# Kernel tuning notes

Measured on AMD Instinct MI355X. Metric: run time of the kernel, lower is better.

The kernel has to match this reference:

```python
import jax, jax.numpy as jnp
import numpy as np

V, E = 50000, 300          # vocab, embedding dim (Word2Vec)
U1, U2, DNS = 256, 256, 128  # lstm1 units, lstm2 units, dense units
B, S = 64, 512             # batch, seq_len


def _glorot(key, shape):
    fan_in, fan_out = shape
    lim = jnp.sqrt(6.0 / (fan_in + fan_out))
    return jax.random.uniform(key, shape, jnp.float32, -lim, lim)


def setup_inputs() -> dict:
    key = jax.random.key(0)
    ks = jax.random.split(key, 12)
    d = {
        'tokens': jax.random.randint(ks[0], (B, S), 0, V),
        'emb': jax.random.normal(ks[1], (V, E), jnp.float32) * 0.05,
        # layer 1 gates: combined dim = E + U1
        'W1f': _glorot(ks[2], (E + U1, U1)), 'b1f': jnp.zeros((U1,), jnp.float32),
        'W1i': _glorot(ks[3], (E + U1, U1)), 'b1i': jnp.zeros((U1,), jnp.float32),
        'W1c': _glorot(ks[4], (E + U1, U1)), 'b1c': jnp.zeros((U1,), jnp.float32),
        'W1o': _glorot(ks[5], (E + U1, U1)), 'b1o': jnp.zeros((U1,), jnp.float32),
        # layer 2 gates: combined dim = U1 + U2
        'W2f': _glorot(ks[6], (U1 + U2, U2)), 'b2f': jnp.zeros((U2,), jnp.float32),
        'W2i': _glorot(ks[7], (U1 + U2, U2)), 'b2i': jnp.zeros((U2,), jnp.float32),
        'W2c': _glorot(ks[8], (U1 + U2, U2)), 'b2c': jnp.zeros((U2,), jnp.float32),
        'W2o': _glorot(ks[9], (U1 + U2, U2)), 'b2o': jnp.zeros((U2,), jnp.float32),
        'Wd': _glorot(ks[10], (U2, DNS)), 'bd': jnp.zeros((DNS,), jnp.float32),
        'Wout': _glorot(ks[11], (DNS, 1)), 'bout': jnp.zeros((1,), jnp.float32),
    }
    return d


def _lstm(x_seq, Wf, bf, Wi, bi, Wc, bc, Wo, bo, units):
    # x_seq: [B, S, D]; scan over time, returns all hidden states [B, S, units]
    b = x_seq.shape[0]
    h0 = jnp.zeros((b, units), x_seq.dtype)
    c0 = jnp.zeros((b, units), x_seq.dtype)

    def step(carry, x_t):
        h, c = carry
        z = jnp.concatenate([x_t, h], axis=-1)           # [B, D+units]
        f = jax.nn.sigmoid(z @ Wf + bf)
        i = jax.nn.sigmoid(z @ Wi + bi)
        g = jnp.tanh(z @ Wc + bc)
        c_new = f * c + i * g
        o = jax.nn.sigmoid(z @ Wo + bo)
        h_new = o * jnp.tanh(c_new)
        return (h_new, c_new), h_new

    (_, _), hs = jax.lax.scan(step, (h0, c0), jnp.swapaxes(x_seq, 0, 1))
    return jnp.swapaxes(hs, 0, 1)  # [B, S, units]


def reference(tokens, emb, W1f, b1f, W1i, b1i, W1c, b1c, W1o, b1o,
              W2f, b2f, W2i, b2i, W2c, b2c, W2o, b2o, Wd, bd, Wout, bout):
    x = emb[tokens]                                       # [B, S, E]
    h1 = _lstm(x, W1f, b1f, W1i, b1i, W1c, b1c, W1o, b1o, U1)   # [B, S, U1]
    h2 = _lstm(h1, W2f, b2f, W2i, b2i, W2c, b2c, W2o, b2o, U2)  # [B, S, U2]
    last = h2[:, -1, :]                                   # return_sequences=False -> final h
    d = jax.nn.relu(last @ Wd + bd)
    return jax.nn.sigmoid(d @ Wout + bout)                # [B, 1]
```

## Files before the change

### kernel.cpp

```cpp
#include <hip/hip_runtime.h>
#include <stdint.h>

typedef __bf16 bf16_t;
typedef __bf16 bf16x8 __attribute__((ext_vector_type(8)));
typedef float floatx16 __attribute__((ext_vector_type(16)));
typedef unsigned int u32;
typedef unsigned long long u64;

#define NPROD 64
#define H1R   8
#define SST   592
#define ZST   1104
#define FP    32

struct KParams {
  const int* tok;
  const float* emb;
  const float* W1[4]; const float* b1[4];
  const float* W2[4]; const float* b2[4];
  const float* Wd; const float* bd; const float* Wout; const float* bout;
  float* out;
  uint16_t* h1;
  uint16_t* h2;
  u32* fl0;
  u32* fl1;
  u32* fl0g;
  u32* pflags;
  float* dstage;
  bf16_t* w1bf;
  float* gx;
  int R;
};

__device__ __forceinline__ float sigf(float x) { return 1.f / (1.f + __expf(-x)); }
__device__ __forceinline__ float tanhf_fast(float x) { return 1.f - 2.f / (__expf(2.f * x) + 1.f); }

__device__ __forceinline__ u32 pack2(float a, float b) {
  uint16_t x = __builtin_bit_cast(uint16_t, (bf16_t)a);
  uint16_t y = __builtin_bit_cast(uint16_t, (bf16_t)b);
  return ((u32)y << 16) | (u32)x;
}
__device__ __forceinline__ float2 u2f2(u64 v) { union { u64 u; float2 f; } x; x.u = v; return x.f; }

__device__ __forceinline__ u32  ald32(const u32* p) { return __hip_atomic_load(p, __ATOMIC_RELAXED, __HIP_MEMORY_SCOPE_AGENT); }
__device__ __forceinline__ void ast32(u32* p, u32 v) { __hip_atomic_store(p, v, __ATOMIC_RELAXED, __HIP_MEMORY_SCOPE_AGENT); }
__device__ __forceinline__ u64  ald64(const u64* p) { return __hip_atomic_load(p, __ATOMIC_RELAXED, __HIP_MEMORY_SCOPE_AGENT); }

template<int NA, int NB>
__device__ __forceinline__ void waitcond(const u32* fa, u32 na, const u32* fb, u32 nb,
                                         const u32* pc, u32 nc) {
  const int lane = threadIdx.x & 63;
  const u32* ap; u32 need;
  if (lane < NA)           { ap = fa + lane * FP;        need = na; }
  else if (lane < NA + NB) { ap = fb + (lane - NA) * FP; need = nb; }
  else                     { ap = pc;                    need = nc; }
  while (!__all(ald32(ap) >= need)) {}
  __atomic_signal_fence(__ATOMIC_ACQUIRE);
}

__device__ __forceinline__ void waitg16(const u32* fa, u32 na) {
  const int lane = threadIdx.x & 63;
  const u32* ap = fa + (lane & 15) * FP;
  while (!__all(ald32(ap) >= na)) {}
  __atomic_signal_fence(__ATOMIC_ACQUIRE);
}

__device__ __forceinline__ void stage_h64(const u64* hp, char* smem) {
  const int tid = threadIdx.x;
  u64 tmp[16];
#pragma unroll
  for (int t = 0; t < 16; ++t) tmp[t] = ald64(hp + tid + 256 * t);
#pragma unroll
  for (int t = 0; t < 16; ++t) {
    int i = tid + 256 * t, b = i >> 6, cc = i & 63;
    *(u64*)(smem + b * SST + cc * 8) = tmp[t];
  }
}

__device__ void run_l0(const KParams& p, int sub, char* abuf, float* cst, float* biasl)
{
  const int tid = threadIdx.x;
  const int w = tid >> 6, l = tid & 63, q = l >> 5, lr = l & 31;
  const int mh = w & 1, nh = w >> 1;

  if (tid < 64) biasl[tid] = p.b1[tid >> 4][sub * 16 + (tid & 15)];

  const int c = nh * 32 + lr;
  const float* Wg = p.W1[c >> 4];
  const int un = sub * 16 + (c & 15);
  bf16x8 wf[16];
#pragma unroll
  for (int s = 0; s < 16; ++s)
#pragma unroll
    for (int j = 0; j < 8; ++j) {
      int k = 16 * s + 8 * q + j;
      wf[s][j] = (bf16_t)Wg[(300 + k) * 256 + un];
    }
  __syncthreads();

  float cs[2][2] = {{0.f, 0.f}, {0.f, 0.f}};

  for (int s = 0; s < 512; ++s) {
    u32 n1 = (s >= 8) ? (u32)(s - 7) : 0u;
    if (w == 0) waitcond<16, 32>(p.fl0, (u32)s, p.fl1, n1, &p.pflags[s * FP], 1u);
    __syncthreads();

    const float* slab = p.gx + (size_t)(s % p.R) * 65536u;
    u64 g[2][4];
#pragma unroll
    for (int kk = 0; kk < 2; ++kk) {
      int pp = tid + 256 * kk, b = pp >> 3, u2 = (pp & 7) * 2;
      const float* gb = slab + b * 1024 + sub * 64 + u2;
      g[kk][0] = ald64((const u64*)gb);
      g[kk][1] = ald64((const u64*)(gb + 16));
      g[kk][2] = ald64((const u64*)(gb + 32));
      g[kk][3] = ald64((const u64*)(gb + 48));
    }
    stage_h64((const u64*)(p.h1 + ((s + H1R - 1) & (H1R - 1)) * 16384), abuf);
    __syncthreads();

    floatx16 acc;
#pragma unroll
    for (int e = 0; e < 16; ++e) acc[e] = 0.f;
    const char* arow = abuf + (mh * 32 + lr) * SST + q * 16;
#pragma unroll
    for (int s2 = 0; s2 < 16; ++s2) {
      bf16x8 af = *(const bf16x8*)(arow + 32 * s2);
      acc = __builtin_amdgcn_mfma_f32_32x32x16_bf16(af, wf[s2], acc, 0, 0, 0);
    }
#pragma unroll
    for (int e = 0; e < 16; ++e) {
      int ri = (e & 3) + 8 * (e >> 2) + 4 * q;
      cst[(mh * 32 + ri) * 68 + nh * 32 + lr] = acc[e];
    }
    __syncthreads();

    uint16_t* hout = p.h1 + (s & (H1R - 1)) * 16384;
#pragma unroll
    for (int kk = 0; kk < 2; ++kk) {
      int pp = tid + 256 * kk, b = pp >> 3, u2 = (pp & 7) * 2;
      float2 pf = *(float2*)&cst[b * 68 +      u2];
      float2 pi = *(float2*)&cst[b * 68 + 16 + u2];
      float2 pg = *(float2*)&cst[b * 68 + 32 + u2];
      float2 po = *(float2*)&cst[b * 68 + 48 + u2];
      float2 gf = u2f2(g[kk][0]), gi = u2f2(g[kk][1]);
      float2 gg = u2f2(g[kk][2]), go = u2f2(g[kk][3]);
      float hv[2];
#pragma unroll
      for (int j = 0; j < 2; ++j) {
        float fj = sigf((j ? pf.y : pf.x) + (j ? gf.y : gf.x) + biasl[u2 + j]);
        float ij = sigf((j ? pi.y : pi.x) + (j ? gi.y : gi.x) + biasl[16 + u2 + j]);
        float gj = tanhf_fast((j ? pg.y : pg.x) + (j ? gg.y : gg.x) + biasl[32 + u2 + j]);
        float oj = sigf((j ? po.y : po.x) + (j ? go.y : go.x) + biasl[48 + u2 + j]);
        float cn = fj * cs[kk][j] + ij * gj;
        cs[kk][j] = cn;
        hv[j] = oj * tanhf_fast(cn);
      }
      ast32((u32*)(hout + b * 256 + sub * 16 + u2), pack2(hv[0], hv[1]));
    }
    __syncthreads();
    if (tid == 0) {
      ast32(&p.fl0[sub * FP], (u32)(s + 1));
      ast32(&p.fl0g[sub * FP], (u32)(s + 1));
    }
  }
}

__device__ void run_l1(const KParams& p, int w2, char* zbuf, float* cst, float* biasl)
{
  const int tid = threadIdx.x;
  const int wv = tid >> 6, l = tid & 63, q = l >> 5, lr = l & 31;
  const int nh = wv & 1, kh = wv >> 1;
  const int bh = w2 & 1, sub1 = w2 >> 1;

  if (tid < 64) biasl[tid] = p.b2[tid >> 4][sub1 * 16 + (tid & 15)];

  const int c = nh * 32 + lr;
  const float* Wg = p.W2[c >> 4];
  const int un = sub1 * 16 + (c & 15);
  bf16x8 wf[16];
#pragma unroll
  for (int s = 0; s < 16; ++s)
#pragma unroll
    for (int j = 0; j < 8; ++j) {
      int k = kh * 256 + s * 16 + q * 8 + j;
      wf[s][j] = (bf16_t)Wg[k * 256 + un];
    }
  __syncthreads();

  float cs2[2] = {0.f, 0.f};
  const int cb = tid >> 3, cu = (tid & 7) * 2;

  for (int s = 0; s < 512; ++s) {
    if (wv == 0) waitcond<32, 16>(p.fl1, (u32)s, p.fl0, (u32)(s + 1), p.fl0, 0u);
    __syncthreads();

    const u64* hp1 = (const u64*)(p.h1 + (s & (H1R - 1)) * 16384) + bh * 2048;
    const u64* hp2 = (const u64*)(p.h2 + ((s + 1) & 1) * 16384) + bh * 2048;
    u64 t1[8], t2[8];
#pragma unroll
    for (int t = 0; t < 8; ++t) t1[t] = ald64(hp1 + tid + 256 * t);
#pragma unroll
    for (int t = 0; t < 8; ++t) t2[t] = ald64(hp2 + tid + 256 * t);
#pragma unroll
    for (int t = 0; t < 8; ++t) {
      int i = tid + 256 * t, r = i >> 6, cc = i & 63;
      *(u64*)(zbuf + r * ZST + cc * 8) = t1[t];
    }
#pragma unroll
    for (int t = 0; t < 8; ++t) {
      int i = tid + 256 * t, r = i >> 6, cc = i & 63;
      *(u64*)(zbuf + r * ZST + 512 + cc * 8) = t2[t];
    }
    __syncthreads();

    floatx16 acc;
#pragma unroll
    for (int e = 0; e < 16; ++e) acc[e] = 0.f;
    const char* arow = zbuf + lr * ZST + kh * 512 + q * 16;
#pragma unroll
    for (int s2 = 0; s2 < 16; ++s2) {
      bf16x8 af = *(const bf16x8*)(arow + 32 * s2);
      acc = __builtin_amdgcn_mfma_f32_32x32x16_bf16(af, wf[s2], acc, 0, 0, 0);
    }
#pragma unroll
    for (int e = 0; e < 16; ++e) {
      int ri = (e & 3) + 8 * (e >> 2) + 4 * q;
      cst[kh * 2176 + ri * 68 + nh * 32 + lr] = acc[e];
    }
    __syncthreads();

    uint16_t* hout = p.h2 + (s & 1) * 16384;
    {
      float2 pf = *(float2*)&cst[cb * 68 +      cu];
      float2 pi = *(float2*)&cst[cb * 68 + 16 + cu];
      float2 pg = *(float2*)&cst[cb * 68 + 32 + cu];
      float2 po = *(float2*)&cst[cb * 68 + 48 + cu];
      float2 qf = *(float2*)&cst[2176 + cb * 68 +      cu];
      float2 qi = *(float2*)&cst[2176 + cb * 68 + 16 + cu];
      float2 qg = *(float2*)&cst[2176 + cb * 68 + 32 + cu];
      float2 qo = *(float2*)&cst[2176 + cb * 68 + 48 + cu];
      float hv[2];
#pragma unroll
      for (int j = 0; j < 2; ++j) {
        float fj = sigf((j ? pf.y + qf.y : pf.x + qf.x) + biasl[cu + j]);
        float ij = sigf((j ? pi.y + qi.y : pi.x + qi.x) + biasl[16 + cu + j]);
        float gj = tanhf_fast((j ? pg.y + qg.y : pg.x + qg.x) + biasl[32 + cu + j]);
        float oj = sigf((j ? po.y + qo.y : po.x + qo.x) + biasl[48 + cu + j]);
        float cn = fj * cs2[j] + ij * gj;
        cs2[j] = cn;
        hv[j] = oj * tanhf_fast(cn);
      }
      ast32((u32*)(hout + (bh * 32 + cb) * 256 + sub1 * 16 + cu), pack2(hv[0], hv[1]));
    }
    __syncthreads();
    if (tid == 0) ast32(&p.fl1[w2 * FP], (u32)(s + 1));
  }

  if (wv == 0) waitcond<32, 0>(p.fl1, 512u, p.fl1, 0u, p.fl1, 0u);
  __syncthreads();
  {
    const u64* hp = (const u64*)(p.h2 + 16384);
    u64 tmp[16];
#pragma unroll
    for (int t = 0; t < 16; ++t) tmp[t] = ald64(hp + tid + 256 * t);
#pragma unroll
    for (int t = 0; t < 16; ++t) {
      int i = tid + 256 * t, b = i >> 6, cc = i & 63;
      *(u64*)(zbuf + b * 520 + cc * 8) = tmp[t];
    }
  }
  __syncthreads();
  {
    int b = tid >> 2, cc = w2 * 4 + (tid & 3);
    const bf16_t* hrow = (const bf16_t*)(zbuf + b * 520);
    float a = p.bd[cc];
#pragma unroll 8
    for (int k = 0; k < 256; ++k) a += (float)hrow[k] * p.Wd[k * 128 + cc];
    ast32((u32*)&p.dstage[b * 128 + cc], __builtin_bit_cast(u32, fmaxf(a, 0.f)));
  }
  __syncthreads();
  if (tid == 0) ast32(&p.fl1[w2 * FP], 513u);

  if (w2 == 0) {
    if (wv == 0) waitcond<32, 0>(p.fl1, 513u, p.fl1, 0u, p.fl1, 0u);
    __syncthreads();
    if (tid < 64) {
      float a = p.bout[0];
#pragma unroll 8
      for (int cc = 0; cc < 128; ++cc) {
        u32 dv = ald32((u32*)&p.dstage[tid * 128 + cc]);
        a += __builtin_bit_cast(float, dv) * p.Wout[cc];
      }
      p.out[tid] = sigf(a);
    }
  }
}

__device__ void run_prod(const KParams& p, int pw, char* smem)
{
  const int tid = threadIdx.x;
  const int w = tid >> 6, l = tid & 63, q = l >> 5, lr = l & 31;
  const int mh = w & 1, chalf = w >> 1;
  const int R = p.R;

  for (int jj = 0; jj < 512 / NPROD; ++jj) {
    const int s = pw + NPROD * jj;
    if (s >= R) {
      if (w == 0) waitg16(p.fl0g, (u32)(s - R + 1));
    }
    __syncthreads();
    {
      int b = tid >> 2, qq = tid & 3;
      int tokv = p.tok[b * 512 + s];
      const float4* src = (const float4*)(p.emb + (size_t)tokv * 300);
      char* dst = smem + b * 656;
      for (int j2 = qq; j2 < 75; j2 += 4) {
        float4 v = src[j2];
        *(u32*)(dst + 8 * j2)     = pack2(v.x, v.y);
        *(u32*)(dst + 8 * j2 + 4) = pack2(v.z, v.w);
      }
      for (int i = tid; i < 640; i += 256) {
        int bb = i / 10, cc2 = i % 10;
        *(u32*)(smem + bb * 656 + 600 + cc2 * 4) = 0u;
      }
    }
    __syncthreads();

    bf16x8 afr[20];
    const char* arow = smem + (mh * 32 + lr) * 656 + q * 16;
#pragma unroll
    for (int kt = 0; kt < 20; ++kt) afr[kt] = *(const bf16x8*)(arow + 32 * kt);

    float* slab = p.gx + (size_t)(s % R) * 65536u;
    for (int c2 = 0; c2 < 16; ++c2) {
      int n = (chalf * 16 + c2) * 32 + lr;
      floatx16 acc;
#pragma unroll
      for (int e = 0; e < 16; ++e) acc[e] = 0.f;
#pragma unroll
      for (int kt = 0; kt < 20; ++kt) {
        bf16x8 bf = ((const bf16x8*)p.w1bf)[(kt * 1024 + n) * 2 + q];
        acc = __builtin_amdgcn_mfma_f32_32x32x16_bf16(afr[kt], bf, acc, 0, 0, 0);
      }
#pragma unroll
      for (int e = 0; e < 16; ++e) {
        int ri = (e & 3) + 8 * (e >> 2) + 4 * q;
        ast32((u32*)(slab + (mh * 32 + ri) * 1024 + n), __builtin_bit_cast(u32, acc[e]));
      }
    }
    __syncthreads();
    if (tid == 0) ast32(&p.pflags[s * FP], 1u);
  }
}

__global__ __launch_bounds__(256, 1) void lstm_main(KParams p)
{
  __shared__ __align__(16) char smem[64 * 656];
  __shared__ float cst[4352];
  __shared__ float biasl[64];
  const int wg = blockIdx.x;
  if (wg < 16)       run_l0(p, wg, smem, cst, biasl);
  else if (wg < 48)  run_l1(p, wg - 16, smem, cst, biasl);
  else               run_prod(p, wg - 48, smem);
}

__global__ void prep_w(KParams p) {
  int idx = blockIdx.x * 256 + threadIdx.x;
  if (idx >= 20 * 1024 * 16) return;
  int kk = idx & 15, n = (idx >> 4) & 1023, kt = idx >> 14;
  int k = kt * 16 + kk;
  int g = (n >> 4) & 3, su = n >> 6, u = n & 15;
  float v = (k < 300) ? p.W1[g][k * 256 + su * 16 + u] : 0.f;
  p.w1bf[idx] = (bf16_t)v;
}

__global__ void init_ws(u32* ws32) {
  int i = blockIdx.x * 256 + threadIdx.x;
  if (i < 100352) ws32[i] = 0u;
}

extern "C" void kernel_launch(void* const* d_in, const int* in_sizes, int n_in,
                              void* d_out, int out_size, void* d_ws, size_t ws_size,
                              hipStream_t stream)
{
  KParams p;
  p.tok = (const int*)d_in[0];
  p.emb = (const float*)d_in[1];
  for (int g = 0; g < 4; ++g) {
    p.W1[g] = (const float*)d_in[2 + 2 * g];
    p.b1[g] = (const float*)d_in[3 + 2 * g];
    p.W2[g] = (const float*)d_in[10 + 2 * g];
    p.b2[g] = (const float*)d_in[11 + 2 * g];
  }
  p.Wd   = (const float*)d_in[18];
  p.bd   = (const float*)d_in[19];
  p.Wout = (const float*)d_in[20];
  p.bout = (const float*)d_in[21];
  p.out  = (float*)d_out;

  char* ws = (char*)d_ws;
  p.h1     = (uint16_t*)ws;
  p.h2     = (uint16_t*)(ws + 262144);
  p.fl0    = (u32*)(ws + 327680);
  p.fl1    = (u32*)(ws + 329728);
  p.fl0g   = (u32*)(ws + 333824);
  p.pflags = (u32*)(ws + 335872);
  p.dstage = (float*)(ws + 401408);
  p.w1bf   = (bf16_t*)(ws + 434176);
  p.gx     = (float*)(ws + 1089536);

  long avail = (long)ws_size - 1089536L;
  int R = (int)(avail / 262144L);
  if (R > 64) R = 64;
  if (R < 1)  R = 1;
  p.R = R;

  hipLaunchKernelGGL(init_ws, dim3(392), dim3(256), 0, stream, (u32*)d_ws);
  hipLaunchKernelGGL(prep_w, dim3(1280), dim3(256), 0, stream, p);
  hipLaunchKernelGGL(lstm_main, dim3(16 + 32 + NPROD), dim3(256), 0, stream, p);
}
```

Baseline: 1.842 ms.

## Load MFMA A-fragments directly from global and store gx in fragment layout

The recurrent LSTM workgroups no longer stage h1/h2 through shared memory. Each lane now loads its own MFMA A-fragment straight from global memory, which removes a staging pass and a barrier per timestep. The producer now writes gate pre-activations in MFMA accumulator order using 64-bit stores, so layer 0 can add them and the bias directly into the accumulator. The h1 ring grows from 8 to 16 slots, which loosens the coupling between layer 0 and layer 1, at the cost of more workspace and redundant uncoalesced global reads per wave.

Result: slower. 3.592 ms (+95.0%).

```diff
diff --git a/kernel.cpp b/kernel.cpp
--- a/kernel.cpp
+++ b/kernel.cpp
@@ -8,9 +8,7 @@
 typedef unsigned long long u64;
 
 #define NPROD 64
-#define H1R   8
-#define SST   592
-#define ZST   1104
+#define H1R   16
 #define FP    32
 
 struct KParams {
@@ -41,10 +39,15 @@
   return ((u32)y << 16) | (u32)x;
 }
 __device__ __forceinline__ float2 u2f2(u64 v) { union { u64 u; float2 f; } x; x.u = v; return x.f; }
+__device__ __forceinline__ u64 f22u(float a, float b) { union { u64 u; float2 f; } x; x.f = make_float2(a, b); return x.u; }
+__device__ __forceinline__ bf16x8 mk_frag(u64 lo, u64 hi) {
+  union { u64 u[2]; bf16x8 v; } x; x.u[0] = lo; x.u[1] = hi; return x.v;
+}
 
 __device__ __forceinline__ u32  ald32(const u32* p) { return __hip_atomic_load(p, __ATOMIC_RELAXED, __HIP_MEMORY_SCOPE_AGENT); }
 __device__ __forceinline__ void ast32(u32* p, u32 v) { __hip_atomic_store(p, v, __ATOMIC_RELAXED, __HIP_MEMORY_SCOPE_AGENT); }
 __device__ __forceinline__ u64  ald64(const u64* p) { return __hip_atomic_load(p, __ATOMIC_RELAXED, __HIP_MEMORY_SCOPE_AGENT); }
+__device__ __forceinline__ void ast64(u64* p, u64 v) { __hip_atomic_store(p, v, __ATOMIC_RELAXED, __HIP_MEMORY_SCOPE_AGENT); }
 
 template<int NA, int NB>
 __device__ __forceinline__ void waitcond(const u32* fa, u32 na, const u32* fb, u32 nb,
@@ -65,29 +68,16 @@
   __atomic_signal_fence(__ATOMIC_ACQUIRE);
 }
 
-__device__ __forceinline__ void stage_h64(const u64* hp, char* smem) {
-  const int tid = threadIdx.x;
-  u64 tmp[16];
-#pragma unroll
-  for (int t = 0; t < 16; ++t) tmp[t] = ald64(hp + tid + 256 * t);
-#pragma unroll
-  for (int t = 0; t < 16; ++t) {
-    int i = tid + 256 * t, b = i >> 6, cc = i & 63;
-    *(u64*)(smem + b * SST + cc * 8) = tmp[t];
-  }
-}
-
-__device__ void run_l0(const KParams& p, int sub, char* abuf, float* cst, float* biasl)
+__device__ void run_l0(const KParams& p, int sub, float* cst)
 {
   const int tid = threadIdx.x;
   const int w = tid >> 6, l = tid & 63, q = l >> 5, lr = l & 31;
   const int mh = w & 1, nh = w >> 1;
 
-  if (tid < 64) biasl[tid] = p.b1[tid >> 4][sub * 16 + (tid & 15)];
-
   const int c = nh * 32 + lr;
   const float* Wg = p.W1[c >> 4];
   const int un = sub * 16 + (c & 15);
+  const float bias = p.b1[c >> 4][un];
   bf16x8 wf[16];
 #pragma unroll
   for (int s = 0; s < 16; ++s)
@@ -96,37 +86,40 @@
       int k = 16 * s + 8 * q + j;
       wf[s][j] = (bf16_t)Wg[(300 + k) * 256 + un];
     }
-  __syncthreads();
 
   float cs[2][2] = {{0.f, 0.f}, {0.f, 0.f}};
+  const int arow64 = (mh * 32 + lr) * 64 + q * 2;
 
   for (int s = 0; s < 512; ++s) {
-    u32 n1 = (s >= 8) ? (u32)(s - 7) : 0u;
-    if (w == 0) waitcond<16, 32>(p.fl0, (u32)s, p.fl1, n1, &p.pflags[s * FP], 1u);
-    __syncthreads();
-
-    const float* slab = p.gx + (size_t)(s % p.R) * 65536u;
-    u64 g[2][4];
-#pragma unroll
-    for (int kk = 0; kk < 2; ++kk) {
-      int pp = tid + 256 * kk, b = pp >> 3, u2 = (pp & 7) * 2;
-      const float* gb = slab + b * 1024 + sub * 64 + u2;
-      g[kk][0] = ald64((const u64*)gb);
-      g[kk][1] = ald64((const u64*)(gb + 16));
-      g[kk][2] = ald64((const u64*)(gb + 32));
-      g[kk][3] = ald64((const u64*)(gb + 48));
-    }
-    stage_h64((const u64*)(p.h1 + ((s + H1R - 1) & (H1R - 1)) * 16384), abuf);
-    __syncthreads();
+    u32 n1 = (s >= H1R) ? (u32)(s - (H1R - 1)) : 0u;
+    if (w == 0) waitcond<16, 16>(p.fl0, (u32)s, p.fl1, n1, &p.pflags[s * FP], 1u);
+    __syncthreads();
+
+    const u64* hp = (const u64*)(p.h1 + ((s + H1R - 1) & (H1R - 1)) * 16384);
+    u64 a0[16], a1[16];
+#pragma unroll
+    for (int s2 = 0; s2 < 16; ++s2) {
+      a0[s2] = ald64(hp + arow64 + s2 * 4);
+      a1[s2] = ald64(hp + arow64 + s2 * 4 + 1);
+    }
+    const float* gb = p.gx + (size_t)(s % p.R) * 65536u
+                    + (size_t)(((sub * 2 + nh) * 2 + mh) * 64 + l) * 16u;
+    u64 gv[8];
+#pragma unroll
+    for (int t = 0; t < 8; ++t) gv[t] = ald64((const u64*)gb + t);
 
     floatx16 acc;
 #pragma unroll
     for (int e = 0; e < 16; ++e) acc[e] = 0.f;
-    const char* arow = abuf + (mh * 32 + lr) * SST + q * 16;
-#pragma unroll
-    for (int s2 = 0; s2 < 16; ++s2) {
-      bf16x8 af = *(const bf16x8*)(arow + 32 * s2);
-      acc = __builtin_amdgcn_mfma_f32_32x32x16_bf16(af, wf[s2], acc, 0, 0, 0);
+#pragma unroll
+    for (int s2 = 0; s2 < 16; ++s2)
+      acc = __builtin_amdgcn_mfma_f32_32x32x16_bf16(mk_frag(a0[s2], a1[s2]), wf[s2], acc, 0, 0, 0);
+
+#pragma unroll
+    for (int t = 0; t < 8; ++t) {
+      float2 f2 = u2f2(gv[t]);
+      acc[2 * t]     += f2.x + bias;
+      acc[2 * t + 1] += f2.y + bias;
     }
 #pragma unroll
     for (int e = 0; e < 16; ++e) {
@@ -143,15 +136,13 @@
       float2 pi = *(float2*)&cst[b * 68 + 16 + u2];
       float2 pg = *(float2*)&cst[b * 68 + 32 + u2];
       float2 po = *(float2*)&cst[b * 68 + 48 + u2];
-      float2 gf = u2f2(g[kk][0]), gi = u2f2(g[kk][1]);
-      float2 gg = u2f2(g[kk][2]), go = u2f2(g[kk][3]);
       float hv[2];
 #pragma unroll
       for (int j = 0; j < 2; ++j) {
-        float fj = sigf((j ? pf.y : pf.x) + (j ? gf.y : gf.x) + biasl[u2 + j]);
-        float ij = sigf((j ? pi.y : pi.x) + (j ? gi.y : gi.x) + biasl[16 + u2 + j]);
-        float gj = tanhf_fast((j ? pg.y : pg.x) + (j ? gg.y : gg.x) + biasl[32 + u2 + j]);
-        float oj = sigf((j ? po.y : po.x) + (j ? go.y : go.x) + biasl[48 + u2 + j]);
+        float fj = sigf(j ? pf.y : pf.x);
+        float ij = sigf(j ? pi.y : pi.x);
+        float gj = tanhf_fast(j ? pg.y : pg.x);
+        float oj = sigf(j ? po.y : po.x);
         float cn = fj * cs[kk][j] + ij * gj;
         cs[kk][j] = cn;
         hv[j] = oj * tanhf_fast(cn);
@@ -166,18 +157,17 @@
   }
 }
 
-__device__ void run_l1(const KParams& p, int w2, char* zbuf, float* cst, float* biasl)
+__device__ void run_l1(const KParams& p, int w2, float* cst)
 {
   const int tid = threadIdx.x;
   const int wv = tid >> 6, l = tid & 63, q = l >> 5, lr = l & 31;
   const int nh = wv & 1, kh = wv >> 1;
   const int bh = w2 & 1, sub1 = w2 >> 1;
 
-  if (tid < 64) biasl[tid] = p.b2[tid >> 4][sub1 * 16 + (tid & 15)];
-
   const int c = nh * 32 + lr;
   const float* Wg = p.W2[c >> 4];
   const int un = sub1 * 16 + (c & 15);
+  const float bias = (kh == 0) ? p.b2[c >> 4][un] : 0.f;
   bf16x8 wf[16];
 #pragma unroll
   for (int s = 0; s < 16; ++s)
@@ -186,47 +176,35 @@
       int k = kh * 256 + s * 16 + q * 8 + j;
       wf[s][j] = (bf16_t)Wg[k * 256 + un];
     }
-  __syncthreads();
 
   float cs2[2] = {0.f, 0.f};
   const int cb = tid >> 3, cu = (tid & 7) * 2;
+  const int arow64 = (bh * 32 + lr) * 64 + q * 2;
 
   for (int s = 0; s < 512; ++s) {
     if (wv == 0) waitcond<32, 16>(p.fl1, (u32)s, p.fl0, (u32)(s + 1), p.fl0, 0u);
     __syncthreads();
 
-    const u64* hp1 = (const u64*)(p.h1 + (s & (H1R - 1)) * 16384) + bh * 2048;
-    const u64* hp2 = (const u64*)(p.h2 + ((s + 1) & 1) * 16384) + bh * 2048;
-    u64 t1[8], t2[8];
-#pragma unroll
-    for (int t = 0; t < 8; ++t) t1[t] = ald64(hp1 + tid + 256 * t);
-#pragma unroll
-    for (int t = 0; t < 8; ++t) t2[t] = ald64(hp2 + tid + 256 * t);
-#pragma unroll
-    for (int t = 0; t < 8; ++t) {
-      int i = tid + 256 * t, r = i >> 6, cc = i & 63;
-      *(u64*)(zbuf + r * ZST + cc * 8) = t1[t];
-    }
-#pragma unroll
-    for (int t = 0; t < 8; ++t) {
-      int i = tid + 256 * t, r = i >> 6, cc = i & 63;
-      *(u64*)(zbuf + r * ZST + 512 + cc * 8) = t2[t];
-    }
-    __syncthreads();
+    const u64* hp = (kh == 0)
+        ? (const u64*)(p.h1 + (s & (H1R - 1)) * 16384)
+        : (const u64*)(p.h2 + ((s + 1) & 1) * 16384);
+    u64 a0[16], a1[16];
+#pragma unroll
+    for (int s2 = 0; s2 < 16; ++s2) {
+      a0[s2] = ald64(hp + arow64 + s2 * 4);
+      a1[s2] = ald64(hp + arow64 + s2 * 4 + 1);
+    }
 
     floatx16 acc;
 #pragma unroll
     for (int e = 0; e < 16; ++e) acc[e] = 0.f;
-    const char* arow = zbuf + lr * ZST + kh * 512 + q * 16;
-#pragma unroll
-    for (int s2 = 0; s2 < 16; ++s2) {
-      bf16x8 af = *(const bf16x8*)(arow + 32 * s2);
-      acc = __builtin_amdgcn_mfma_f32_32x32x16_bf16(af, wf[s2], acc, 0, 0, 0);
-    }
+#pragma unroll
+    for (int s2 = 0; s2 < 16; ++s2)
+      acc = __builtin_amdgcn_mfma_f32_32x32x16_bf16(mk_frag(a0[s2], a1[s2]), wf[s2], acc, 0, 0, 0);
 #pragma unroll
     for (int e = 0; e < 16; ++e) {
       int ri = (e & 3) + 8 * (e >> 2) + 4 * q;
-      cst[kh * 2176 + ri * 68 + nh * 32 + lr] = acc[e];
+      cst[kh * 2176 + ri * 68 + nh * 32 + lr] = acc[e] + bias;
     }
     __syncthreads();
 
@@ -243,10 +221,10 @@
       float hv[2];
 #pragma unroll
       for (int j = 0; j < 2; ++j) {
-        float fj = sigf((j ? pf.y + qf.y : pf.x + qf.x) + biasl[cu + j]);
-        float ij = sigf((j ? pi.y + qi.y : pi.x + qi.x) + biasl[16 + cu + j]);
-        float gj = tanhf_fast((j ? pg.y + qg.y : pg.x + qg.x) + biasl[32 + cu + j]);
-        float oj = sigf((j ? po.y + qo.y : po.x + qo.x) + biasl[48 + cu + j]);
+        float fj = sigf(j ? pf.y + qf.y : pf.x + qf.x);
+        float ij = sigf(j ? pi.y + qi.y : pi.x + qi.x);
+        float gj = tanhf_fast(j ? pg.y + qg.y : pg.x + qg.x);
+        float oj = sigf(j ? po.y + qo.y : po.x + qo.x);
         float cn = fj * cs2[j] + ij * gj;
         cs2[j] = cn;
         hv[j] = oj * tanhf_fast(cn);
@@ -267,13 +245,13 @@
 #pragma unroll
     for (int t = 0; t < 16; ++t) {
       int i = tid + 256 * t, b = i >> 6, cc = i & 63;
-      *(u64*)(zbuf + b * 520 + cc * 8) = tmp[t];
+      *(u64*)((char*)cst + b * 520 + cc * 8) = tmp[t];
     }
   }
   __syncthreads();
   {
     int b = tid >> 2, cc = w2 * 4 + (tid & 3);
-    const bf16_t* hrow = (const bf16_t*)(zbuf + b * 520);
+    const bf16_t* hrow = (const bf16_t*)((char*)cst + b * 520);
     float a = p.bd[cc];
 #pragma unroll 8
     for (int k = 0; k < 256; ++k) a += (float)hrow[k] * p.Wd[k * 128 + cc];
@@ -334,7 +312,8 @@
 
     float* slab = p.gx + (size_t)(s % R) * 65536u;
     for (int c2 = 0; c2 < 16; ++c2) {
-      int n = (chalf * 16 + c2) * 32 + lr;
+      int ct = chalf * 16 + c2;
+      int n = ct * 32 + lr;
       floatx16 acc;
 #pragma unroll
       for (int e = 0; e < 16; ++e) acc[e] = 0.f;
@@ -343,11 +322,9 @@
         bf16x8 bf = ((const bf16x8*)p.w1bf)[(kt * 1024 + n) * 2 + q];
         acc = __builtin_amdgcn_mfma_f32_32x32x16_bf16(afr[kt], bf, acc, 0, 0, 0);
       }
-#pragma unroll
-      for (int e = 0; e < 16; ++e) {
-        int ri = (e & 3) + 8 * (e >> 2) + 4 * q;
-        ast32((u32*)(slab + (mh * 32 + ri) * 1024 + n), __builtin_bit_cast(u32, acc[e]));
-      }
+      u64* gout = (u64*)(slab + (size_t)((ct * 2 + mh) * 64 + l) * 16u);
+#pragma unroll
+      for (int t = 0; t < 8; ++t) ast64(gout + t, f22u(acc[2 * t], acc[2 * t + 1]));
     }
     __syncthreads();
     if (tid == 0) ast32(&p.pflags[s * FP], 1u);
@@ -358,10 +335,9 @@
 {
   __shared__ __align__(16) char smem[64 * 656];
   __shared__ float cst[4352];
-  __shared__ float biasl[64];
   const int wg = blockIdx.x;
-  if (wg < 16)       run_l0(p, wg, smem, cst, biasl);
-  else if (wg < 48)  run_l1(p, wg - 16, smem, cst, biasl);
+  if (wg < 16)       run_l0(p, wg, cst);
+  else if (wg < 48)  run_l1(p, wg - 16, cst);
   else               run_prod(p, wg - 48, smem);
 }
 
@@ -377,7 +353,7 @@
 
 __global__ void init_ws(u32* ws32) {
   int i = blockIdx.x * 256 + threadIdx.x;
-  if (i < 100352) ws32[i] = 0u;
+  if (i < 165888) ws32[i] = 0u;
 }
 
 extern "C" void kernel_launch(void* const* d_in, const int* in_sizes, int n_in,
@@ -401,22 +377,22 @@
 
   char* ws = (char*)d_ws;
   p.h1     = (uint16_t*)ws;
-  p.h2     = (uint16_t*)(ws + 262144);
-  p.fl0    = (u32*)(ws + 327680);
-  p.fl1    = (u32*)(ws + 329728);
-  p.fl0g   = (u32*)(ws + 333824);
-  p.pflags = (u32*)(ws + 335872);
-  p.dstage = (float*)(ws + 401408);
-  p.w1bf   = (bf16_t*)(ws + 434176);
-  p.gx     = (float*)(ws + 1089536);
-
-  long avail = (long)ws_size - 1089536L;
+  p.h2     = (uint16_t*)(ws + 524288);
+  p.fl0    = (u32*)(ws + 589824);
+  p.fl1    = (u32*)(ws + 591872);
+  p.fl0g   = (u32*)(ws + 595968);
+  p.pflags = (u32*)(ws + 598016);
+  p.dstage = (float*)(ws + 663552);
+  p.w1bf   = (bf16_t*)(ws + 696320);
+  p.gx     = (float*)(ws + 1351680);
+
+  long avail = (long)ws_size - 1351680L;
   int R = (int)(avail / 262144L);
   if (R > 64) R = 64;
   if (R < 1)  R = 1;
   p.R = R;
 
-  hipLaunchKernelGGL(init_ws, dim3(392), dim3(256), 0, stream, (u32*)d_ws);
+  hipLaunchKernelGGL(init_ws, dim3(648), dim3(256), 0, stream, (u32*)d_ws);
   hipLaunchKernelGGL(prep_w, dim3(1280), dim3(256), 0, stream, p);
   hipLaunchKernelGGL(lstm_main, dim3(16 + 32 + NPROD), dim3(256), 0, stream, p);
 }
```
